# Kernel tuning notes

Measured on AMD Instinct MI355X. Metric: run time of the kernel, lower is better.

Reference implementation:

```python
import jax, jax.numpy as jnp
import numpy as np

B, S1, S2, D = 16, 2048, 2048, 1024
H = D // 2  # 512


def setup_inputs() -> dict:
    key = jax.random.key(0)
    ks = jax.random.split(key, 12)
    s = lambda fan_in: 1.0 / np.sqrt(fan_in)
    return {
        "features1": jax.random.normal(ks[0], (B, S1, D), jnp.float32),
        "features2": jax.random.normal(ks[1], (B, S2, D), jnp.float32),
        "Wq": jax.random.uniform(ks[2], (H, D), jnp.float32, -s(D), s(D)),
        "bq": jax.random.uniform(ks[3], (H,), jnp.float32, -s(D), s(D)),
        "Wk": jax.random.uniform(ks[4], (H, D), jnp.float32, -s(D), s(D)),
        "bk": jax.random.uniform(ks[5], (H,), jnp.float32, -s(D), s(D)),
        "Wv": jax.random.uniform(ks[6], (H, D), jnp.float32, -s(D), s(D)),
        "bv": jax.random.uniform(ks[7], (H,), jnp.float32, -s(D), s(D)),
        "Wc1": jax.random.uniform(ks[8], (H, D), jnp.float32, -s(D), s(D)),
        "bc1": jax.random.uniform(ks[9], (H,), jnp.float32, -s(D), s(D)),
        "Wc2": jax.random.uniform(ks[10], (1, H), jnp.float32, -s(H), s(H)),
        "bc2": jax.random.uniform(ks[11], (1,), jnp.float32, -s(H), s(H)),
    }


def reference(features1, features2, Wq, bq, Wk, bk, Wv, bv, Wc1, bc1, Wc2, bc2):
    # Projections: (B,S,D) @ (D,H) -> (B,S,H)
    q = jnp.einsum("bsd,hd->bsh", features1, Wq) + bq
    k = jnp.einsum("btd,hd->bth", features2, Wk) + bk
    v = jnp.einsum("btd,hd->bth", features2, Wv) + bv
    # Single-head cross attention, scale = sqrt(D//2)
    scores = jnp.einsum("bsh,bth->bst", q, k) / jnp.sqrt(jnp.float32(q.shape[-1]))
    attn = jax.nn.softmax(scores, axis=-1)
    attended = jnp.einsum("bst,bth->bsh", attn, v)
    # Concat + mean pool over segments
    fused = jnp.concatenate([q, attended], axis=-1)  # (B,S1,D)
    pooled = fused.mean(axis=1)  # (B,D)
    # Classifier MLP (dropout is identity at inference)
    h = jax.nn.relu(pooled @ Wc1.T + bc1)
    return h @ Wc2.T + bc2  # (B,1)
```

## Files before the change

### kernel.cpp

```cpp
#include <hip/hip_runtime.h>
#include <stdint.h>

#define NB   16
#define NS   2048
#define ND   1024
#define NH   512
#define SCALE 0.044194173824159216f

typedef __attribute__((ext_vector_type(4))) float f32x4;
typedef __attribute__((ext_vector_type(8))) short s16x8;

__device__ __forceinline__ short f2bf(float f) {
  __bf16 h = (__bf16)f;
  return __builtin_bit_cast(short, h);
}

__device__ __forceinline__ void gl_lds16(const void* g, void* l) {
  __builtin_amdgcn_global_load_lds(
      (const __attribute__((address_space(1))) void*)g,
      (__attribute__((address_space(3))) void*)l, 16, 0, 0);
}

#define MFMA16(a, b, c) __builtin_amdgcn_mfma_f32_16x16x32_bf16((a), (b), (c), 0, 0, 0)

__global__ __launch_bounds__(256) void cvt_f32_bf16(const float* __restrict__ src,
                                                    short* __restrict__ dst, int n) {
  int i = (blockIdx.x * 256 + threadIdx.x) * 8;
  if (i + 7 < n) {
    f32x4 a = *(const f32x4*)(src + i);
    f32x4 b = *(const f32x4*)(src + i + 4);
    s16x8 o;
    o[0] = f2bf(a[0]); o[1] = f2bf(a[1]); o[2] = f2bf(a[2]); o[3] = f2bf(a[3]);
    o[4] = f2bf(b[0]); o[5] = f2bf(b[1]); o[6] = f2bf(b[2]); o[7] = f2bf(b[3]);
    *(s16x8*)(dst + i) = o;
  }
}

__global__ __launch_bounds__(256) void proj_kernel(const float* __restrict__ X,
                                                   const short* __restrict__ Wb,
                                                   const float* __restrict__ bias,
                                                   short* __restrict__ out) {
  const int m0 = blockIdx.x * 32;
  const int tid = threadIdx.x;
  const int lane = tid & 63;
  const int wid = tid >> 6;

  __shared__ short At[32 * 64];
  __shared__ short Bt[512 * 64];

  f32x4 acc[2][8] = {};

  const int ar = tid >> 3;
  const int agk = (tid & 7) * 8;

  for (int kt = 0; kt < 16; ++kt) {
    __syncthreads();
    {
      const float* sp = X + (long)(m0 + ar) * ND + kt * 64 + agk;
      f32x4 a = *(const f32x4*)sp;
      f32x4 b = *(const f32x4*)(sp + 4);
      s16x8 o;
      o[0] = f2bf(a[0]); o[1] = f2bf(a[1]); o[2] = f2bf(a[2]); o[3] = f2bf(a[3]);
      o[4] = f2bf(b[0]); o[5] = f2bf(b[1]); o[6] = f2bf(b[2]); o[7] = f2bf(b[3]);
      int off = (ar * 128 + agk * 2) ^ ((ar & 7) << 4);
      *(s16x8*)((char*)At + off) = o;
    }
    {
      const char* wb = (const char*)Wb;
      for (int i = 0; i < 16; ++i) {
        int p = (i * 256 + tid) * 16;
        int row = p >> 7;
        long gsrc = (long)row * 2048 + kt * 128 + ((p & 127) ^ ((row & 7) << 4));
        gl_lds16(wb + gsrc, (char*)Bt + i * 4096 + wid * 1024);
      }
    }
    asm volatile("s_waitcnt vmcnt(0)" ::: "memory");
    __syncthreads();
#pragma unroll
    for (int kk = 0; kk < 2; ++kk) {
      const int kofs = (kk * 32 + (lane >> 4) * 8) * 2;
      s16x8 af[2], bfr[8];
#pragma unroll
      for (int i = 0; i < 2; ++i) {
        int r = i * 16 + (lane & 15);
        int off = (r * 128 + kofs) ^ ((r & 7) << 4);
        af[i] = *(const s16x8*)((const char*)At + off);
      }
#pragma unroll
      for (int j = 0; j < 8; ++j) {
        int r = wid * 128 + j * 16 + (lane & 15);
        int off = (r * 128 + kofs) ^ ((r & 7) << 4);
        bfr[j] = *(const s16x8*)((const char*)Bt + off);
      }
#pragma unroll
      for (int i = 0; i < 2; ++i)
#pragma unroll
        for (int j = 0; j < 8; ++j) acc[i][j] = MFMA16(af[i], bfr[j], acc[i][j]);
    }
  }
#pragma unroll
  for (int j = 0; j < 8; ++j) {
    int col = wid * 128 + j * 16 + (lane & 15);
    float bv = bias[col];
#pragma unroll
    for (int i = 0; i < 2; ++i) {
      int rbase = m0 + i * 16 + ((lane >> 4) & 3) * 4;
#pragma unroll
      for (int r = 0; r < 4; ++r) {
        out[(long)(rbase + r) * NH + col] = f2bf(acc[i][j][r] + bv);
      }
    }
  }
}

__global__ __launch_bounds__(256) void attn_rowsum(const short* __restrict__ qb,
                                                   const short* __restrict__ kb,
                                                   float* __restrict__ rl) {
  const int b = blockIdx.y, sblk = blockIdx.x;
  const int tid = threadIdx.x, lane = tid & 63, wid = tid >> 6;
  const int srow = sblk * 64 + wid * 16;

  __shared__ short Kt[64 * 512];

  s16x8 qf[16];
  {
    const short* qp = qb + (long)(b * NS + srow + (lane & 15)) * NH + (lane >> 4) * 8;
#pragma unroll
    for (int kk = 0; kk < 16; ++kk) qf[kk] = *(const s16x8*)(qp + kk * 32);
  }

  float part[4] = {0.f, 0.f, 0.f, 0.f};
  const char* kbase = (const char*)(kb + (long)b * NS * NH);

  for (int tt = 0; tt < 32; ++tt) {
    __syncthreads();
    const char* tb = kbase + (long)tt * 64 * 1024;
    for (int i = 0; i < 16; ++i) {
      int p = (i * 256 + tid) * 16;
      int src = p ^ (((p >> 10) & 7) << 4);
      gl_lds16(tb + src, (char*)Kt + i * 4096 + wid * 1024);
    }
    asm volatile("s_waitcnt vmcnt(0)" ::: "memory");
    __syncthreads();

    f32x4 acc[4] = {};
#pragma unroll
    for (int kk = 0; kk < 16; ++kk) {
      const int kofs = (kk * 32 + (lane >> 4) * 8) * 2;
#pragma unroll
      for (int cf = 0; cf < 4; ++cf) {
        int t = cf * 16 + (lane & 15);
        int off = (t * 1024 + kofs) ^ ((t & 7) << 4);
        s16x8 bfr = *(const s16x8*)((const char*)Kt + off);
        acc[cf] = MFMA16(qf[kk], bfr, acc[cf]);
      }
    }
#pragma unroll
    for (int cf = 0; cf < 4; ++cf)
#pragma unroll
      for (int r = 0; r < 4; ++r) part[r] += __expf(acc[cf][r] * SCALE);
  }

#pragma unroll
  for (int m = 1; m < 16; m <<= 1)
#pragma unroll
    for (int r = 0; r < 4; ++r) part[r] += __shfl_xor(part[r], m, 64);

  if ((lane & 15) == 0) {
    int g = lane >> 4;
#pragma unroll
    for (int r = 0; r < 4; ++r)
      rl[b * NS + srow + g * 4 + r] = 1.0f / part[r];
  }
}

__global__ __launch_bounds__(256) void attn_colsum(const short* __restrict__ qb,
                                                   const short* __restrict__ kb,
                                                   const float* __restrict__ rl,
                                                   float* __restrict__ w) {
  const int b = blockIdx.y, tblk = blockIdx.x;
  const int tid = threadIdx.x, lane = tid & 63, wid = tid >> 6;
  const int trow = tblk * 64 + wid * 16;

  __shared__ short Qt[64 * 512];

  s16x8 kf[16];
  {
    const short* kp = kb + (long)(b * NS + trow + (lane & 15)) * NH + (lane >> 4) * 8;
#pragma unroll
    for (int kk = 0; kk < 16; ++kk) kf[kk] = *(const s16x8*)(kp + kk * 32);
  }

  float part[4] = {0.f, 0.f, 0.f, 0.f};
  const char* qbase = (const char*)(qb + (long)b * NS * NH);
  const float* rlb = rl + b * NS;

  for (int ss = 0; ss < 32; ++ss) {
    __syncthreads();
    const char* sb = qbase + (long)ss * 64 * 1024;
    for (int i = 0; i < 16; ++i) {
      int p = (i * 256 + tid) * 16;
      int src = p ^ (((p >> 10) & 7) << 4);
      gl_lds16(sb + src, (char*)Qt + i * 4096 + wid * 1024);
    }
    asm volatile("s_waitcnt vmcnt(0)" ::: "memory");
    __syncthreads();

    f32x4 acc[4] = {};
#pragma unroll
    for (int kk = 0; kk < 16; ++kk) {
      const int kofs = (kk * 32 + (lane >> 4) * 8) * 2;
#pragma unroll
      for (int cf = 0; cf < 4; ++cf) {
        int s = cf * 16 + (lane & 15);
        int off = (s * 1024 + kofs) ^ ((s & 7) << 4);
        s16x8 bfr = *(const s16x8*)((const char*)Qt + off);
        acc[cf] = MFMA16(kf[kk], bfr, acc[cf]);
      }
    }
#pragma unroll
    for (int cf = 0; cf < 4; ++cf) {
      float rv = rlb[ss * 64 + cf * 16 + (lane & 15)];
#pragma unroll
      for (int r = 0; r < 4; ++r) part[r] += __expf(acc[cf][r] * SCALE) * rv;
    }
  }

#pragma unroll
  for (int m = 1; m < 16; m <<= 1)
#pragma unroll
    for (int r = 0; r < 4; ++r) part[r] += __shfl_xor(part[r], m, 64);

  if ((lane & 15) == 0) {
    int g = lane >> 4;
#pragma unroll
    for (int r = 0; r < 4; ++r)
      w[b * NS + trow + g * 4 + r] = part[r];
  }
}

__global__ __launch_bounds__(256) void colmean(const float* __restrict__ f1,
                                               float* __restrict__ mf1) {
  int d = blockIdx.x * 256 + threadIdx.x;
  int b = blockIdx.z;
  long base = ((long)b * NS + blockIdx.y * 128) * ND + d;
  float acc = 0.f;
  for (int s = 0; s < 128; ++s) acc += f1[base + (long)s * ND];
  atomicAdd(&mf1[b * ND + d], acc * (1.0f / 2048.0f));
}

__global__ __launch_bounds__(256) void weighted_colsum(const float* __restrict__ f2,
                                                       const float* __restrict__ w,
                                                       float* __restrict__ g) {
  int d = blockIdx.x * 256 + threadIdx.x;
  int b = blockIdx.z;
  int t0 = blockIdx.y * 128;
  long base = ((long)b * NS + t0) * ND + d;
  const float* wr = w + b * NS + t0;
  float acc = 0.f;
  for (int t = 0; t < 128; ++t) acc += wr[t] * f2[base + (long)t * ND];
  atomicAdd(&g[b * ND + d], acc);
}

__global__ __launch_bounds__(512) void final_mlp(
    const float* __restrict__ mf1, const float* __restrict__ g,
    const float* __restrict__ Wq, const float* __restrict__ bq,
    const float* __restrict__ Wv, const float* __restrict__ bv,
    const float* __restrict__ Wc1, const float* __restrict__ bc1,
    const float* __restrict__ Wc2, const float* __restrict__ bc2,
    float* __restrict__ out) {
  const int b = blockIdx.x;
  const int j = threadIdx.x;
  __shared__ float pooled[1024];
  __shared__ float red[8];

  const f32x4* m4 = (const f32x4*)(mf1 + b * ND);
  const f32x4* g4 = (const f32x4*)(g + b * ND);
  const f32x4* wq4 = (const f32x4*)(Wq + (long)j * ND);
  const f32x4* wv4 = (const f32x4*)(Wv + (long)j * ND);
  float mq = 0.f, av = 0.f;
  for (int i = 0; i < 256; ++i) {
    f32x4 a = m4[i], x = wq4[i];
    mq += a[0] * x[0] + a[1] * x[1] + a[2] * x[2] + a[3] * x[3];
    f32x4 c = g4[i], y = wv4[i];
    av += c[0] * y[0] + c[1] * y[1] + c[2] * y[2] + c[3] * y[3];
  }
  pooled[j] = mq + bq[j];
  pooled[512 + j] = av * (1.0f / 2048.0f) + bv[j];
  __syncthreads();

  const f32x4* p4 = (const f32x4*)pooled;
  const f32x4* wc4 = (const f32x4*)(Wc1 + (long)j * ND);
  float h = bc1[j];
  for (int i = 0; i < 256; ++i) {
    f32x4 p = p4[i], y = wc4[i];
    h += p[0] * y[0] + p[1] * y[1] + p[2] * y[2] + p[3] * y[3];
  }
  h = fmaxf(h, 0.f) * Wc2[j];

#pragma unroll
  for (int m = 1; m < 64; m <<= 1) h += __shfl_xor(h, m, 64);
  if ((j & 63) == 0) red[j >> 6] = h;
  __syncthreads();
  if (j == 0) {
    float t = 0.f;
#pragma unroll
    for (int k = 0; k < 8; ++k) t += red[k];
    out[b] = t + bc2[0];
  }
}

extern "C" void kernel_launch(void* const* d_in, const int* in_sizes, int n_in,
                              void* d_out, int out_size, void* d_ws, size_t ws_size,
                              hipStream_t stream) {
  const float* f1 = (const float*)d_in[0];
  const float* f2 = (const float*)d_in[1];
  const float* Wq = (const float*)d_in[2];
  const float* bq = (const float*)d_in[3];
  const float* Wk = (const float*)d_in[4];
  const float* bk = (const float*)d_in[5];
  const float* Wv = (const float*)d_in[6];
  const float* bv = (const float*)d_in[7];
  const float* Wc1 = (const float*)d_in[8];
  const float* bc1 = (const float*)d_in[9];
  const float* Wc2 = (const float*)d_in[10];
  const float* bc2 = (const float*)d_in[11];
  float* out = (float*)d_out;

  char* ws = (char*)d_ws;
  short* qbuf = (short*)ws;
  short* kbuf = (short*)(ws + (32l << 20));
  short* Wqb = (short*)(ws + (64l << 20));
  short* Wkb = (short*)(ws + (65l << 20));
  float* rl = (float*)(ws + (66l << 20));
  float* wbuf = (float*)(ws + (66l << 20) + (128l << 10));
  float* mf1 = (float*)(ws + (66l << 20) + (256l << 10));
  float* gbuf = (float*)(ws + (66l << 20) + (320l << 10));

  hipMemsetAsync(mf1, 0, NB * ND * sizeof(float), stream);
  hipMemsetAsync(gbuf, 0, NB * ND * sizeof(float), stream);

  cvt_f32_bf16<<<256, 256, 0, stream>>>(Wq, Wqb, NH * ND);
  cvt_f32_bf16<<<256, 256, 0, stream>>>(Wk, Wkb, NH * ND);

  proj_kernel<<<NB * NS / 32, 256, 0, stream>>>(f1, Wqb, bq, qbuf);
  proj_kernel<<<NB * NS / 32, 256, 0, stream>>>(f2, Wkb, bk, kbuf);

  attn_rowsum<<<dim3(NS / 64, NB), 256, 0, stream>>>(qbuf, kbuf, rl);
  attn_colsum<<<dim3(NS / 64, NB), 256, 0, stream>>>(qbuf, kbuf, rl, wbuf);

  colmean<<<dim3(4, 16, 16), 256, 0, stream>>>(f1, mf1);
  weighted_colsum<<<dim3(4, 16, 16), 256, 0, stream>>>(f2, wbuf, gbuf);

  final_mlp<<<NB, 512, 0, stream>>>(mf1, gbuf, Wq, bq, Wv, bv, Wc1, bc1, Wc2,
                                    bc2, out);
}
```

Baseline: 805.7 us.

## Store exp scores once to skip recomputing QK^T for column sums

Adds a path that computes QK^T once, writes the unnormalised exponentials in bf16 to a transposed P buffer, and accumulates row sums with atomics. A separate pass then takes reciprocals and reduces each P column against them to get the attention weight sums, so the second QK^T pass is no longer needed. It also splits the final MLP into two wider kernels so more blocks work in parallel. The cost is writing and re-reading a 128 MB buffer, and the path only runs if the workspace is large enough; exp is not max-subtracted, so it relies on the scores staying small.

Result: faster. 733.4 us (-9.0%).

```diff
diff --git a/kernel.cpp b/kernel.cpp
--- a/kernel.cpp
+++ b/kernel.cpp
@@ -9,10 +9,15 @@
 
 typedef __attribute__((ext_vector_type(4))) float f32x4;
 typedef __attribute__((ext_vector_type(8))) short s16x8;
+typedef __attribute__((ext_vector_type(4))) short s16x4;
 
 __device__ __forceinline__ short f2bf(float f) {
   __bf16 h = (__bf16)f;
   return __builtin_bit_cast(short, h);
+}
+__device__ __forceinline__ float bf2f(short s) {
+  unsigned int u = ((unsigned int)(unsigned short)s) << 16;
+  return __builtin_bit_cast(float, u);
 }
 
 __device__ __forceinline__ void gl_lds16(const void* g, void* l) {
@@ -111,6 +116,117 @@
       }
     }
   }
+}
+
+__global__ __launch_bounds__(256) void attn_rowsum_p(const short* __restrict__ qb,
+                                                     const short* __restrict__ kb,
+                                                     float* __restrict__ rsum,
+                                                     short* __restrict__ Pt) {
+  const int sblk = blockIdx.x, thalf = blockIdx.y, b = blockIdx.z;
+  const int tid = threadIdx.x, lane = tid & 63, wid = tid >> 6;
+  const int s0 = sblk * 128 + wid * 32;
+
+  __shared__ short Kt[64 * 512];
+
+  s16x8 qf[2][16];
+#pragma unroll
+  for (int i = 0; i < 2; ++i) {
+    const short* qp = qb + (long)(b * NS + s0 + i * 16 + (lane & 15)) * NH + (lane >> 4) * 8;
+#pragma unroll
+    for (int kk = 0; kk < 16; ++kk) qf[i][kk] = *(const s16x8*)(qp + kk * 32);
+  }
+
+  float part[2][4] = {};
+  const char* kbase = (const char*)(kb + (long)b * NS * NH) + (long)thalf * 1024 * 1024;
+
+  for (int tt = 0; tt < 16; ++tt) {
+    __syncthreads();
+    const char* tb = kbase + (long)tt * 64 * 1024;
+    for (int i = 0; i < 16; ++i) {
+      int p = (i * 256 + tid) * 16;
+      int src = p ^ (((p >> 10) & 7) << 4);
+      gl_lds16(tb + src, (char*)Kt + i * 4096 + wid * 1024);
+    }
+    asm volatile("s_waitcnt vmcnt(0)" ::: "memory");
+    __syncthreads();
+
+    f32x4 acc[2][4] = {};
+#pragma unroll
+    for (int kk = 0; kk < 16; ++kk) {
+      const int kofs = (kk * 32 + (lane >> 4) * 8) * 2;
+      s16x8 bfr[4];
+#pragma unroll
+      for (int cf = 0; cf < 4; ++cf) {
+        int t = cf * 16 + (lane & 15);
+        int off = (t * 1024 + kofs) ^ ((t & 7) << 4);
+        bfr[cf] = *(const s16x8*)((const char*)Kt + off);
+      }
+#pragma unroll
+      for (int i = 0; i < 2; ++i)
+#pragma unroll
+        for (int cf = 0; cf < 4; ++cf) acc[i][cf] = MFMA16(qf[i][kk], bfr[cf], acc[i][cf]);
+    }
+
+#pragma unroll
+    for (int i = 0; i < 2; ++i)
+#pragma unroll
+      for (int cf = 0; cf < 4; ++cf) {
+        s16x4 pw;
+        float e0 = __expf(acc[i][cf][0] * SCALE);
+        float e1 = __expf(acc[i][cf][1] * SCALE);
+        float e2 = __expf(acc[i][cf][2] * SCALE);
+        float e3 = __expf(acc[i][cf][3] * SCALE);
+        part[i][0] += e0; part[i][1] += e1; part[i][2] += e2; part[i][3] += e3;
+        pw[0] = f2bf(e0); pw[1] = f2bf(e1); pw[2] = f2bf(e2); pw[3] = f2bf(e3);
+        int t = thalf * 1024 + tt * 64 + cf * 16 + (lane & 15);
+        long s_base = s0 + i * 16 + (lane >> 4) * 4;
+        *(s16x4*)(Pt + (long)(b * NS + t) * NS + s_base) = pw;
+      }
+  }
+
+#pragma unroll
+  for (int m = 1; m < 16; m <<= 1)
+#pragma unroll
+    for (int i = 0; i < 2; ++i)
+#pragma unroll
+      for (int r = 0; r < 4; ++r) part[i][r] += __shfl_xor(part[i][r], m, 64);
+
+  if ((lane & 15) == 0) {
+#pragma unroll
+    for (int i = 0; i < 2; ++i)
+#pragma unroll
+      for (int r = 0; r < 4; ++r)
+        atomicAdd(&rsum[b * NS + s0 + i * 16 + (lane >> 4) * 4 + r], part[i][r]);
+  }
+}
+
+__global__ __launch_bounds__(256) void recip_kernel(const float* __restrict__ rsum,
+                                                    float* __restrict__ rl) {
+  int i = blockIdx.x * 256 + threadIdx.x;
+  if (i < NB * NS) rl[i] = 1.0f / rsum[i];
+}
+
+__global__ __launch_bounds__(256) void wsum_kernel(const short* __restrict__ Pt,
+                                                   const float* __restrict__ rl,
+                                                   float* __restrict__ w) {
+  int gw = blockIdx.x * 4 + (threadIdx.x >> 6);
+  int lane = threadIdx.x & 63;
+  int b = gw >> 11, t = gw & 2047;
+  const short* pr = Pt + (long)(b * NS + t) * NS + lane * 32;
+  const float* rr = rl + b * NS + lane * 32;
+  float acc = 0.f;
+#pragma unroll
+  for (int c = 0; c < 4; ++c) {
+    s16x8 pv = *(const s16x8*)(pr + c * 8);
+    f32x4 r0 = *(const f32x4*)(rr + c * 8);
+    f32x4 r1 = *(const f32x4*)(rr + c * 8 + 4);
+    acc += bf2f(pv[0]) * r0[0] + bf2f(pv[1]) * r0[1] + bf2f(pv[2]) * r0[2] +
+           bf2f(pv[3]) * r0[3] + bf2f(pv[4]) * r1[0] + bf2f(pv[5]) * r1[1] +
+           bf2f(pv[6]) * r1[2] + bf2f(pv[7]) * r1[3];
+  }
+#pragma unroll
+  for (int m = 1; m < 64; m <<= 1) acc += __shfl_xor(acc, m, 64);
+  if (lane == 0) w[b * NS + t] = acc;
 }
 
 __global__ __launch_bounds__(256) void attn_rowsum(const short* __restrict__ qb,
@@ -262,51 +378,64 @@
   atomicAdd(&g[b * ND + d], acc);
 }
 
-__global__ __launch_bounds__(512) void final_mlp(
+__global__ __launch_bounds__(256) void pooled_kernel(
     const float* __restrict__ mf1, const float* __restrict__ g,
     const float* __restrict__ Wq, const float* __restrict__ bq,
     const float* __restrict__ Wv, const float* __restrict__ bv,
-    const float* __restrict__ Wc1, const float* __restrict__ bc1,
-    const float* __restrict__ Wc2, const float* __restrict__ bc2,
-    float* __restrict__ out) {
-  const int b = blockIdx.x;
-  const int j = threadIdx.x;
-  __shared__ float pooled[1024];
-  __shared__ float red[8];
-
-  const f32x4* m4 = (const f32x4*)(mf1 + b * ND);
-  const f32x4* g4 = (const f32x4*)(g + b * ND);
-  const f32x4* wq4 = (const f32x4*)(Wq + (long)j * ND);
-  const f32x4* wv4 = (const f32x4*)(Wv + (long)j * ND);
-  float mq = 0.f, av = 0.f;
-  for (int i = 0; i < 256; ++i) {
-    f32x4 a = m4[i], x = wq4[i];
-    mq += a[0] * x[0] + a[1] * x[1] + a[2] * x[2] + a[3] * x[3];
-    f32x4 c = g4[i], y = wv4[i];
-    av += c[0] * y[0] + c[1] * y[1] + c[2] * y[2] + c[3] * y[3];
-  }
-  pooled[j] = mq + bq[j];
-  pooled[512 + j] = av * (1.0f / 2048.0f) + bv[j];
-  __syncthreads();
-
-  const f32x4* p4 = (const f32x4*)pooled;
-  const f32x4* wc4 = (const f32x4*)(Wc1 + (long)j * ND);
-  float h = bc1[j];
-  for (int i = 0; i < 256; ++i) {
-    f32x4 p = p4[i], y = wc4[i];
-    h += p[0] * y[0] + p[1] * y[1] + p[2] * y[2] + p[3] * y[3];
-  }
-  h = fmaxf(h, 0.f) * Wc2[j];
-
-#pragma unroll
-  for (int m = 1; m < 64; m <<= 1) h += __shfl_xor(h, m, 64);
-  if ((j & 63) == 0) red[j >> 6] = h;
-  __syncthreads();
-  if (j == 0) {
-    float t = 0.f;
-#pragma unroll
-    for (int k = 0; k < 8; ++k) t += red[k];
-    out[b] = t + bc2[0];
+    float* __restrict__ pooled) {
+  int gw = blockIdx.x * 4 + (threadIdx.x >> 6);
+  int lane = threadIdx.x & 63;
+  const float* wrow;
+  const float* xbase;
+  float bias, scale;
+  if (gw < 512) {
+    wrow = Wq + (long)gw * ND; xbase = mf1; bias = bq[gw]; scale = 1.0f;
+  } else {
+    wrow = Wv + (long)(gw - 512) * ND; xbase = g; bias = bv[gw - 512];
+    scale = 1.0f / 2048.0f;
+  }
+  f32x4 wreg[4];
+#pragma unroll
+  for (int i = 0; i < 4; ++i) wreg[i] = *(const f32x4*)(wrow + i * 256 + lane * 4);
+  for (int b = 0; b < NB; ++b) {
+    const f32x4* x = (const f32x4*)(xbase + (long)b * ND);
+    float p = 0.f;
+#pragma unroll
+    for (int i = 0; i < 4; ++i) {
+      f32x4 xv = x[i * 64 + lane];
+      p += wreg[i][0] * xv[0] + wreg[i][1] * xv[1] + wreg[i][2] * xv[2] + wreg[i][3] * xv[3];
+    }
+#pragma unroll
+    for (int m = 1; m < 64; m <<= 1) p += __shfl_xor(p, m, 64);
+    if (lane == 0) pooled[b * ND + gw] = p * scale + bias;
+  }
+}
+
+__global__ __launch_bounds__(256) void out_kernel(
+    const float* __restrict__ pooled, const float* __restrict__ Wc1,
+    const float* __restrict__ bc1, const float* __restrict__ Wc2,
+    const float* __restrict__ bc2, float* __restrict__ out) {
+  int j = blockIdx.x * 4 + (threadIdx.x >> 6);
+  int lane = threadIdx.x & 63;
+  f32x4 wreg[4];
+#pragma unroll
+  for (int i = 0; i < 4; ++i)
+    wreg[i] = *(const f32x4*)(Wc1 + (long)j * ND + i * 256 + lane * 4);
+  for (int b = 0; b < NB; ++b) {
+    const f32x4* x = (const f32x4*)(pooled + (long)b * ND);
+    float p = 0.f;
+#pragma unroll
+    for (int i = 0; i < 4; ++i) {
+      f32x4 xv = x[i * 64 + lane];
+      p += wreg[i][0] * xv[0] + wreg[i][1] * xv[1] + wreg[i][2] * xv[2] + wreg[i][3] * xv[3];
+    }
+#pragma unroll
+    for (int m = 1; m < 64; m <<= 1) p += __shfl_xor(p, m, 64);
+    if (lane == 0) {
+      float h = fmaxf(p + bc1[j], 0.f) * Wc2[j];
+      if (j == 0) h += bc2[0];
+      atomicAdd(&out[b], h);
+    }
   }
 }
 
@@ -332,13 +461,20 @@
   short* kbuf = (short*)(ws + (32l << 20));
   short* Wqb = (short*)(ws + (64l << 20));
   short* Wkb = (short*)(ws + (65l << 20));
-  float* rl = (float*)(ws + (66l << 20));
-  float* wbuf = (float*)(ws + (66l << 20) + (128l << 10));
-  float* mf1 = (float*)(ws + (66l << 20) + (256l << 10));
-  float* gbuf = (float*)(ws + (66l << 20) + (320l << 10));
+  float* rsum = (float*)(ws + (66l << 20));
+  float* rl = (float*)(ws + (66l << 20) + (128l << 10));
+  float* wbuf = (float*)(ws + (66l << 20) + (256l << 10));
+  float* mf1 = (float*)(ws + (66l << 20) + (384l << 10));
+  float* gbuf = (float*)(ws + (66l << 20) + (448l << 10));
+  float* pooled = (float*)(ws + (66l << 20) + (512l << 10));
+  short* Pt = (short*)(ws + (68l << 20));
+
+  const bool useP = ws_size >= ((68l << 20) + (long)NB * NS * NS * 2);
 
   hipMemsetAsync(mf1, 0, NB * ND * sizeof(float), stream);
   hipMemsetAsync(gbuf, 0, NB * ND * sizeof(float), stream);
+  hipMemsetAsync(out, 0, NB * sizeof(float), stream);
+  if (useP) hipMemsetAsync(rsum, 0, NB * NS * sizeof(float), stream);
 
   cvt_f32_bf16<<<256, 256, 0, stream>>>(Wq, Wqb, NH * ND);
   cvt_f32_bf16<<<256, 256, 0, stream>>>(Wk, Wkb, NH * ND);
@@ -346,12 +482,18 @@
   proj_kernel<<<NB * NS / 32, 256, 0, stream>>>(f1, Wqb, bq, qbuf);
   proj_kernel<<<NB * NS / 32, 256, 0, stream>>>(f2, Wkb, bk, kbuf);
 
-  attn_rowsum<<<dim3(NS / 64, NB), 256, 0, stream>>>(qbuf, kbuf, rl);
-  attn_colsum<<<dim3(NS / 64, NB), 256, 0, stream>>>(qbuf, kbuf, rl, wbuf);
+  if (useP) {
+    attn_rowsum_p<<<dim3(16, 2, NB), 256, 0, stream>>>(qbuf, kbuf, rsum, Pt);
+    recip_kernel<<<NB * NS / 256, 256, 0, stream>>>(rsum, rl);
+    wsum_kernel<<<NB * NS / 4, 256, 0, stream>>>(Pt, rl, wbuf);
+  } else {
+    attn_rowsum<<<dim3(NS / 64, NB), 256, 0, stream>>>(qbuf, kbuf, rl);
+    attn_colsum<<<dim3(NS / 64, NB), 256, 0, stream>>>(qbuf, kbuf, rl, wbuf);
+  }
 
   colmean<<<dim3(4, 16, 16), 256, 0, stream>>>(f1, mf1);
   weighted_colsum<<<dim3(4, 16, 16), 256, 0, stream>>>(f2, wbuf, gbuf);
 
-  final_mlp<<<NB, 512, 0, stream>>>(mf1, gbuf, Wq, bq, Wv, bv, Wc1, bc1, Wc2,
-                                    bc2, out);
-}
+  pooled_kernel<<<256, 256, 0, stream>>>(mf1, gbuf, Wq, bq, Wv, bv, pooled);
+  out_kernel<<<128, 256, 0, stream>>>(pooled, Wc1, bc1, Wc2, bc2, out);
+}
```
